# Kernel optimization log

Hardware: AMD Instinct MI355X
Metric: run time of the kernel (lower is better)

Reference implementation:

```python
import jax, jax.numpy as jnp
import numpy as np
import math

B, S, D, H = 4, 512, 128, 4
HD = D // H
NEG = float(-2**32 + 1)

def _ln(x, g, b, eps=1e-8):
    m = jnp.mean(x, axis=-1, keepdims=True)
    v = jnp.var(x, axis=-1, keepdims=True)
    return (x - m) * jax.lax.rsqrt(v + eps) * g + b

def setup_inputs() -> dict:
    key = jax.random.key(0)
    ks = jax.random.split(key, 16)
    s = 0.02
    inp = {
        'embed': jax.random.normal(ks[0], (B, S, D), jnp.float32),
        'time_matrix_K': jax.random.normal(ks[1], (B, S, S, D), jnp.float32),
        'time_matrix_V': jax.random.normal(ks[2], (B, S, S, D), jnp.float32),
        # causal additive mask: large negative above diagonal (1--mask semantics)
        'attn_mask': jnp.where(jnp.triu(jnp.ones((S, S), bool), k=1), jnp.float32(-1e9), jnp.float32(0.0)),
        'padding_mask': jnp.zeros((B, S), bool),
        'wq': jax.random.normal(ks[3], (D, D), jnp.float32) * s,
        'bq': jnp.zeros((D,), jnp.float32),
        'wk': jax.random.normal(ks[4], (D, D), jnp.float32) * s,
        'bk': jnp.zeros((D,), jnp.float32),
        'wv': jax.random.normal(ks[5], (D, D), jnp.float32) * s,
        'bv': jnp.zeros((D,), jnp.float32),
        'wo': jax.random.normal(ks[6], (D, D), jnp.float32) * s,
        'bo': jnp.zeros((D,), jnp.float32),
        'ln1_g': jnp.ones((D,), jnp.float32),
        'ln1_b': jnp.zeros((D,), jnp.float32),
        'ln2_g': jnp.ones((D,), jnp.float32),
        'ln2_b': jnp.zeros((D,), jnp.float32),
        'w1': jax.random.normal(ks[7], (D, D), jnp.float32) * s,  # d_ff defaults to d_model
        'b1': jnp.zeros((D,), jnp.float32),
        'w2': jax.random.normal(ks[8], (D, D), jnp.float32) * s,
        'b2': jnp.zeros((D,), jnp.float32),
    }
    return inp

def reference(embed, time_matrix_K, time_matrix_V, attn_mask, padding_mask,
              wq, bq, wk, bk, wv, bv, wo, bo,
              ln1_g, ln1_b, ln2_g, ln2_b, w1, b1, w2, b2):
    # Pre-LN on Q only (K, V take raw embed), per original block
    Qn = _ln(embed, ln1_g, ln1_b)
    q = (Qn @ wq + bq).reshape(B, S, H, HD).transpose(0, 2, 1, 3)      # bhqd
    k = (embed @ wk + bk).reshape(B, S, H, HD).transpose(0, 2, 1, 3)   # bhkd
    v = (embed @ wv + bv).reshape(B, S, H, HD).transpose(0, 2, 1, 3)   # bhkd
    tmK = time_matrix_K.reshape(B, S, S, H, HD).transpose(0, 3, 1, 2, 4)  # bhqkd
    tmV = time_matrix_V.reshape(B, S, S, H, HD).transpose(0, 3, 1, 2, 4)  # bhqkd
    scale = math.sqrt(HD)
    energy = jnp.einsum('bhqd,bhkd->bhqk', q, k)
    energy = energy + jnp.einsum('bhqkd,bhqd->bhqk', tmK, q)
    energy = energy / scale
    energy = energy + attn_mask[None, None]
    energy = jnp.where(padding_mask[:, None, None, :], jnp.float32(NEG), energy)
    attn = jax.nn.softmax(energy, axis=-1)  # dropout is identity in eval
    O = jnp.einsum('bhqk,bhkd->bhqd', attn, v)
    O = O + jnp.einsum('bhqk,bhqkd->bhqd', attn, tmV)
    O = O.transpose(0, 2, 1, 3).reshape(B, S, D)
    O = O @ wo + bo
    x = Qn + O                      # residual adds LN'd Q, per original code
    x = _ln(x, ln2_g, ln2_b)
    ff = jax.nn.gelu(x @ w1 + b1, approximate=False) @ w2 + b2
    return ff + x
```

## Files before the change

### kernel.cpp

```cpp
#include <hip/hip_runtime.h>
#include <math.h>

#define Bsz 4
#define Ssz 512
#define Dsz 128
#define Hsz 4
#define HDsz 32
#define KT 64
#define NT 8

typedef float floatx4 __attribute__((ext_vector_type(4)));

static __device__ __forceinline__ float4 ldnt4(const float* p) {
    floatx4 v = __builtin_nontemporal_load(reinterpret_cast<const floatx4*>(p));
    float4 r; r.x = v.x; r.y = v.y; r.z = v.z; r.w = v.w;
    return r;
}

__global__ __launch_bounds__(128) void k_pre(
    const float* __restrict__ embed,
    const float* __restrict__ wq, const float* __restrict__ bq,
    const float* __restrict__ wk, const float* __restrict__ bk,
    const float* __restrict__ wv, const float* __restrict__ bv,
    const float* __restrict__ g1, const float* __restrict__ b1,
    float* __restrict__ Qn, float* __restrict__ Qs,
    float* __restrict__ Kp, float* __restrict__ Vp)
{
    __shared__ float xs[4][128];
    __shared__ float qs[4][128];
    const int t = threadIdx.x;
    const int row0 = blockIdx.x * 4;
    const int r = t >> 5;
    const int c = t & 31;
    const int d4 = c << 2;

    const float4* e4 = (const float4*)(embed + (size_t)row0 * Dsz);
    float4 x4 = e4[r * 32 + c];

    float s = x4.x + x4.y + x4.z + x4.w;
    #pragma unroll
    for (int o = 1; o < 32; o <<= 1) s += __shfl_xor(s, o);
    const float m = s * (1.0f / 128.0f);

    const float dx0 = x4.x - m, dx1 = x4.y - m, dx2 = x4.z - m, dx3 = x4.w - m;
    float vs = dx0*dx0 + dx1*dx1 + dx2*dx2 + dx3*dx3;
    #pragma unroll
    for (int o = 1; o < 32; o <<= 1) vs += __shfl_xor(vs, o);
    const float rstd = rsqrtf(vs * (1.0f / 128.0f) + 1e-8f);

    const float4 g4 = *(const float4*)(g1 + d4);
    const float4 bb4 = *(const float4*)(b1 + d4);
    float4 qn4;
    qn4.x = dx0 * rstd * g4.x + bb4.x;
    qn4.y = dx1 * rstd * g4.y + bb4.y;
    qn4.z = dx2 * rstd * g4.z + bb4.z;
    qn4.w = dx3 * rstd * g4.w + bb4.w;

    xs[r][d4+0] = x4.x; xs[r][d4+1] = x4.y; xs[r][d4+2] = x4.z; xs[r][d4+3] = x4.w;
    qs[r][d4+0] = qn4.x; qs[r][d4+1] = qn4.y; qs[r][d4+2] = qn4.z; qs[r][d4+3] = qn4.w;
    *(float4*)(Qn + (size_t)(row0 + r) * Dsz + d4) = qn4;
    __syncthreads();

    float aq[4] = {0,0,0,0}, ak[4] = {0,0,0,0}, av[4] = {0,0,0,0};
    for (int d = 0; d < 128; ++d) {
        const float wqv = wq[d*128 + t];
        const float wkv = wk[d*128 + t];
        const float wvv = wv[d*128 + t];
        #pragma unroll
        for (int rr = 0; rr < 4; ++rr) {
            aq[rr] += qs[rr][d] * wqv;
            ak[rr] += xs[rr][d] * wkv;
            av[rr] += xs[rr][d] * wvv;
        }
    }
    const float inv_scale = 0.17677669529663687f;
    const float bqv = bq[t], bkv = bk[t], bvv = bv[t];
    #pragma unroll
    for (int rr = 0; rr < 4; ++rr) {
        const size_t o = (size_t)(row0 + rr) * Dsz + t;
        Qs[o] = (aq[rr] + bqv) * inv_scale;
        Kp[o] = ak[rr] + bkv;
        Vp[o] = av[rr] + bvv;
    }
}

__global__ __launch_bounds__(256) void k_attn_tile(
    const float* __restrict__ tmK, const float* __restrict__ tmV,
    const float* __restrict__ Qs, const float* __restrict__ Kp,
    const float* __restrict__ Vp,
    float* __restrict__ Opart,
    float* __restrict__ ml)
{
    const int id = blockIdx.x;
    const int b = id & 3;
    const int q = (id >> 2) & (Ssz - 1);
    const int tile = id >> 11;
    const int k0 = tile * KT;
    if (k0 > q) return;

    const int t = threadIdx.x;
    const int w = t >> 6;
    const int lane = t & 63;
    const int rg = lane >> 3;
    const int fs = lane & 7;
    const int d4 = w * HDsz + fs * 4;

    const int nr_full = q - k0 + 1;
    const int nr = nr_full > KT ? KT : nr_full;
    const size_t rowq = (size_t)(b * Ssz + q);

    const float4 q4 = *(const float4*)(Qs + rowq * Dsz + d4);
    const float* tmKb = tmK + (rowq * (size_t)Ssz + k0) * Dsz;
    const float* Kb   = Kp + ((size_t)b * Ssz + k0) * Dsz;

    float p[8];
    #pragma unroll
    for (int i0 = 0; i0 < 8; i0 += 4) {
        float4 a[4], kv[4];
        #pragma unroll
        for (int u = 0; u < 4; ++u) {
            const int r = (i0 + u) * 8 + rg;
            if (r < nr) {
                a[u]  = ldnt4(tmKb + (size_t)r * Dsz + d4);
                kv[u] = *(const float4*)(Kb + (size_t)r * Dsz + d4);
            } else {
                a[u] = make_float4(0,0,0,0); kv[u] = make_float4(0,0,0,0);
            }
        }
        #pragma unroll
        for (int u = 0; u < 4; ++u) {
            const int r = (i0 + u) * 8 + rg;
            float val = q4.x*(a[u].x+kv[u].x) + q4.y*(a[u].y+kv[u].y)
                      + q4.z*(a[u].z+kv[u].z) + q4.w*(a[u].w+kv[u].w);
            val += __shfl_xor(val, 1);
            val += __shfl_xor(val, 2);
            val += __shfl_xor(val, 4);
            p[i0 + u] = (r < nr) ? val : -INFINITY;
        }
    }

    float mx = p[0];
    #pragma unroll
    for (int i = 1; i < 8; ++i) mx = fmaxf(mx, p[i]);
    mx = fmaxf(mx, __shfl_xor(mx, 8));
    mx = fmaxf(mx, __shfl_xor(mx, 16));
    mx = fmaxf(mx, __shfl_xor(mx, 32));

    float lsum = 0.0f;
    #pragma unroll
    for (int i = 0; i < 8; ++i) {
        p[i] = __expf(p[i] - mx);
        lsum += p[i];
    }
    lsum += __shfl_xor(lsum, 8);
    lsum += __shfl_xor(lsum, 16);
    lsum += __shfl_xor(lsum, 32);

    if (lane == 0) {
        float* mlp = ml + ((rowq * NT + tile) * Hsz + w) * 2;
        mlp[0] = mx;
        mlp[1] = lsum;
    }

    const float* tmVb = tmV + (rowq * (size_t)Ssz + k0) * Dsz;
    const float* Vb   = Vp + ((size_t)b * Ssz + k0) * Dsz;
    float4 acc = {0.0f, 0.0f, 0.0f, 0.0f};
    #pragma unroll
    for (int i0 = 0; i0 < 8; i0 += 4) {
        float4 a[4], vv[4];
        #pragma unroll
        for (int u = 0; u < 4; ++u) {
            const int r = (i0 + u) * 8 + rg;
            if (r < nr) {
                a[u]  = ldnt4(tmVb + (size_t)r * Dsz + d4);
                vv[u] = *(const float4*)(Vb + (size_t)r * Dsz + d4);
            } else {
                a[u] = make_float4(0,0,0,0); vv[u] = make_float4(0,0,0,0);
            }
        }
        #pragma unroll
        for (int u = 0; u < 4; ++u) {
            const float pw = p[i0 + u];
            acc.x += pw * (a[u].x + vv[u].x);
            acc.y += pw * (a[u].y + vv[u].y);
            acc.z += pw * (a[u].z + vv[u].z);
            acc.w += pw * (a[u].w + vv[u].w);
        }
    }
    #pragma unroll
    for (int o = 8; o < 64; o <<= 1) {
        acc.x += __shfl_xor(acc.x, o);
        acc.y += __shfl_xor(acc.y, o);
        acc.z += __shfl_xor(acc.z, o);
        acc.w += __shfl_xor(acc.w, o);
    }
    if (lane < 8) {
        float4* op = (float4*)(Opart + (rowq * NT + tile) * Dsz + d4);
        *op = acc;
    }
}

__global__ __launch_bounds__(128) void k_combine(
    const float* __restrict__ Opart, const float* __restrict__ ml,
    float* __restrict__ Oa)
{
    const size_t rowq = blockIdx.x;
    const int q = (int)(rowq & (Ssz - 1));
    const int nt = (q >> 6) + 1;
    const int d = threadIdx.x;
    const int h = d >> 5;

    float M = -INFINITY;
    #pragma unroll 8
    for (int i = 0; i < nt; ++i)
        M = fmaxf(M, ml[((rowq * NT + i) * Hsz + h) * 2 + 0]);

    float den = 0.0f, o = 0.0f;
    #pragma unroll 8
    for (int i = 0; i < nt; ++i) {
        const float* mlp = ml + ((rowq * NT + i) * Hsz + h) * 2;
        const float w = __expf(mlp[0] - M);
        den += w * mlp[1];
        o   += w * Opart[(rowq * NT + i) * Dsz + d];
    }
    Oa[rowq * Dsz + d] = o / den;
}

__global__ __launch_bounds__(128) void k_post(
    const float* __restrict__ Oa, const float* __restrict__ Qn,
    const float* __restrict__ wo, const float* __restrict__ bo,
    const float* __restrict__ g2, const float* __restrict__ b2ln,
    const float* __restrict__ w1, const float* __restrict__ b1,
    const float* __restrict__ w2, const float* __restrict__ b2,
    float* __restrict__ out)
{
    __shared__ float os[4][128];
    __shared__ float xn[4][128];
    __shared__ float hbuf[4][128];
    const int t = threadIdx.x;
    const int row0 = blockIdx.x * 4;
    const int r = t >> 5;
    const int c = t & 31;
    const int d4 = c << 2;

    {
        const float4* o4 = (const float4*)(Oa + (size_t)row0 * Dsz);
        const float4 v = o4[r * 32 + c];
        os[r][d4+0] = v.x; os[r][d4+1] = v.y; os[r][d4+2] = v.z; os[r][d4+3] = v.w;
    }
    __syncthreads();

    float ao[4] = {0,0,0,0};
    for (int d = 0; d < 128; ++d) {
        const float wv = wo[d*128 + t];
        #pragma unroll
        for (int rr = 0; rr < 4; ++rr) ao[rr] += os[rr][d] * wv;
    }
    const float bov = bo[t];
    float xrow[4];
    #pragma unroll
    for (int rr = 0; rr < 4; ++rr)
        xrow[rr] = Qn[(size_t)(row0 + rr) * Dsz + t] + ao[rr] + bov;
    __syncthreads();
    #pragma unroll
    for (int rr = 0; rr < 4; ++rr) os[rr][t] = xrow[rr];
    __syncthreads();

    {
        const float4 x4 = *(const float4*)(&os[r][d4]);
        float s = x4.x + x4.y + x4.z + x4.w;
        #pragma unroll
        for (int o = 1; o < 32; o <<= 1) s += __shfl_xor(s, o);
        const float m = s * (1.0f / 128.0f);
        const float dx0 = x4.x - m, dx1 = x4.y - m, dx2 = x4.z - m, dx3 = x4.w - m;
        float vs = dx0*dx0 + dx1*dx1 + dx2*dx2 + dx3*dx3;
        #pragma unroll
        for (int o = 1; o < 32; o <<= 1) vs += __shfl_xor(vs, o);
        const float rstd = rsqrtf(vs * (1.0f / 128.0f) + 1e-8f);
        const float4 g4 = *(const float4*)(g2 + d4);
        const float4 bb4 = *(const float4*)(b2ln + d4);
        xn[r][d4+0] = dx0 * rstd * g4.x + bb4.x;
        xn[r][d4+1] = dx1 * rstd * g4.y + bb4.y;
        xn[r][d4+2] = dx2 * rstd * g4.z + bb4.z;
        xn[r][d4+3] = dx3 * rstd * g4.w + bb4.w;
    }
    __syncthreads();

    float a1[4] = {0,0,0,0};
    for (int d = 0; d < 128; ++d) {
        const float wv = w1[d*128 + t];
        #pragma unroll
        for (int rr = 0; rr < 4; ++rr) a1[rr] += xn[rr][d] * wv;
    }
    const float b1v = b1[t];
    #pragma unroll
    for (int rr = 0; rr < 4; ++rr) {
        const float hv = a1[rr] + b1v;
        hbuf[rr][t] = 0.5f * hv * (1.0f + erff(hv * 0.70710678118654752f));
    }
    __syncthreads();

    float a2[4] = {0,0,0,0};
    for (int d = 0; d < 128; ++d) {
        const float wv = w2[d*128 + t];
        #pragma unroll
        for (int rr = 0; rr < 4; ++rr) a2[rr] += hbuf[rr][d] * wv;
    }
    const float b2v = b2[t];
    #pragma unroll
    for (int rr = 0; rr < 4; ++rr)
        out[(size_t)(row0 + rr) * Dsz + t] = a2[rr] + b2v + xn[rr][t];
}

extern "C" void kernel_launch(void* const* d_in, const int* in_sizes, int n_in,
                              void* d_out, int out_size, void* d_ws, size_t ws_size,
                              hipStream_t stream) {
    const float* embed = (const float*)d_in[0];
    const float* tmK   = (const float*)d_in[1];
    const float* tmV   = (const float*)d_in[2];
    const float* wq = (const float*)d_in[5];
    const float* bq = (const float*)d_in[6];
    const float* wk = (const float*)d_in[7];
    const float* bk = (const float*)d_in[8];
    const float* wv = (const float*)d_in[9];
    const float* bv = (const float*)d_in[10];
    const float* wo = (const float*)d_in[11];
    const float* bo = (const float*)d_in[12];
    const float* g1 = (const float*)d_in[13];
    const float* b1l = (const float*)d_in[14];
    const float* g2 = (const float*)d_in[15];
    const float* b2l = (const float*)d_in[16];
    const float* w1 = (const float*)d_in[17];
    const float* b1 = (const float*)d_in[18];
    const float* w2 = (const float*)d_in[19];
    const float* b2 = (const float*)d_in[20];

    const size_t NE = (size_t)Bsz * Ssz * Dsz;
    float* ws = (float*)d_ws;
    float* Qn = ws;
    float* Qs = ws + NE;
    float* Kp = ws + 2 * NE;
    float* Vp = ws + 3 * NE;
    float* Oa = ws + 4 * NE;
    float* Opart = ws + 5 * NE;
    float* mlbuf = ws + 5 * NE + (size_t)Bsz * Ssz * NT * Dsz;

    k_pre<<<(Bsz * Ssz) / 4, 128, 0, stream>>>(embed, wq, bq, wk, bk, wv, bv,
                                               g1, b1l, Qn, Qs, Kp, Vp);
    k_attn_tile<<<Bsz * Ssz * NT, 256, 0, stream>>>(tmK, tmV, Qs, Kp, Vp,
                                                    Opart, mlbuf);
    k_combine<<<Bsz * Ssz, 128, 0, stream>>>(Opart, mlbuf, Oa);
    k_post<<<(Bsz * Ssz) / 4, 128, 0, stream>>>(Oa, Qn, wo, bo, g2, b2l,
                                                w1, b1, w2, b2, (float*)d_out);
}
```

Measured before the change: 141.6 us.

## Remap attention tiles to one wave each and fuse split-K combine into post kernel

Each wave now handles a whole (query, key-tile) pair covering all four heads, with lanes spanning the 128-wide feature row and two rows in flight. This lengthens per-lane row loops, adds a fast path with no bounds checks for full tiles, and cuts cross-lane reductions. The separate combine kernel is removed and its log-sum-exp merge moves into k_post, which saves one launch and the Oa round trip. The trade-off is higher register pressure from p[32] and 8-deep load batches, and an early return per wave inside a block could leave idle waves.

```diff
diff --git a/kernel.cpp b/kernel.cpp
--- a/kernel.cpp
+++ b/kernel.cpp
@@ -84,26 +84,24 @@
     }
 }
 
-__global__ __launch_bounds__(256) void k_attn_tile(
+__global__ __launch_bounds__(256, 4) void k_attn_tile(
     const float* __restrict__ tmK, const float* __restrict__ tmV,
     const float* __restrict__ Qs, const float* __restrict__ Kp,
     const float* __restrict__ Vp,
     float* __restrict__ Opart,
     float* __restrict__ ml)
 {
-    const int id = blockIdx.x;
-    const int b = id & 3;
-    const int q = (id >> 2) & (Ssz - 1);
-    const int tile = id >> 11;
+    const int tau = blockIdx.x * 4 + (threadIdx.x >> 6);
+    const int b = tau & 3;
+    const int q = (tau >> 2) & (Ssz - 1);
+    const int tile = tau >> 11;
     const int k0 = tile * KT;
     if (k0 > q) return;
 
-    const int t = threadIdx.x;
-    const int w = t >> 6;
-    const int lane = t & 63;
-    const int rg = lane >> 3;
-    const int fs = lane & 7;
-    const int d4 = w * HDsz + fs * 4;
+    const int lane = threadIdx.x & 63;
+    const int r5 = lane >> 5;
+    const int fs = lane & 31;
+    const int d4 = fs << 2;
 
     const int nr_full = q - k0 + 1;
     const int nr = nr_full > KT ? KT : nr_full;
@@ -113,51 +111,70 @@
     const float* tmKb = tmK + (rowq * (size_t)Ssz + k0) * Dsz;
     const float* Kb   = Kp + ((size_t)b * Ssz + k0) * Dsz;
 
-    float p[8];
-    #pragma unroll
-    for (int i0 = 0; i0 < 8; i0 += 4) {
-        float4 a[4], kv[4];
-        #pragma unroll
-        for (int u = 0; u < 4; ++u) {
-            const int r = (i0 + u) * 8 + rg;
-            if (r < nr) {
-                a[u]  = ldnt4(tmKb + (size_t)r * Dsz + d4);
-                kv[u] = *(const float4*)(Kb + (size_t)r * Dsz + d4);
-            } else {
-                a[u] = make_float4(0,0,0,0); kv[u] = make_float4(0,0,0,0);
-            }
-        }
-        #pragma unroll
-        for (int u = 0; u < 4; ++u) {
-            const int r = (i0 + u) * 8 + rg;
-            float val = q4.x*(a[u].x+kv[u].x) + q4.y*(a[u].y+kv[u].y)
-                      + q4.z*(a[u].z+kv[u].z) + q4.w*(a[u].w+kv[u].w);
-            val += __shfl_xor(val, 1);
-            val += __shfl_xor(val, 2);
-            val += __shfl_xor(val, 4);
-            p[i0 + u] = (r < nr) ? val : -INFINITY;
+    float p[32];
+
+    if (nr == KT) {
+        #pragma unroll
+        for (int c2 = 0; c2 < 4; ++c2) {
+            float4 a[8], kv[8];
+            #pragma unroll
+            for (int jj = 0; jj < 8; ++jj) {
+                const int r = 2*(c2*8 + jj) + r5;
+                a[jj]  = ldnt4(tmKb + (size_t)r * Dsz + d4);
+                kv[jj] = *(const float4*)(Kb + (size_t)r * Dsz + d4);
+            }
+            #pragma unroll
+            for (int jj = 0; jj < 8; ++jj) {
+                float val = q4.x*(a[jj].x+kv[jj].x) + q4.y*(a[jj].y+kv[jj].y)
+                          + q4.z*(a[jj].z+kv[jj].z) + q4.w*(a[jj].w+kv[jj].w);
+                val += __shfl_xor(val, 1);
+                val += __shfl_xor(val, 2);
+                val += __shfl_xor(val, 4);
+                p[c2*8 + jj] = val;
+            }
+        }
+    } else {
+        #pragma unroll
+        for (int c2 = 0; c2 < 4; ++c2) {
+            float4 a[8], kv[8];
+            #pragma unroll
+            for (int jj = 0; jj < 8; ++jj) {
+                const int r = 2*(c2*8 + jj) + r5;
+                if (r < nr) {
+                    a[jj]  = ldnt4(tmKb + (size_t)r * Dsz + d4);
+                    kv[jj] = *(const float4*)(Kb + (size_t)r * Dsz + d4);
+                } else {
+                    a[jj] = make_float4(0,0,0,0); kv[jj] = make_float4(0,0,0,0);
+                }
+            }
+            #pragma unroll
+            for (int jj = 0; jj < 8; ++jj) {
+                const int r = 2*(c2*8 + jj) + r5;
+                float val = q4.x*(a[jj].x+kv[jj].x) + q4.y*(a[jj].y+kv[jj].y)
+                          + q4.z*(a[jj].z+kv[jj].z) + q4.w*(a[jj].w+kv[jj].w);
+                val += __shfl_xor(val, 1);
+                val += __shfl_xor(val, 2);
+                val += __shfl_xor(val, 4);
+                p[c2*8 + jj] = (r < nr) ? val : -INFINITY;
+            }
         }
     }
 
     float mx = p[0];
     #pragma unroll
-    for (int i = 1; i < 8; ++i) mx = fmaxf(mx, p[i]);
-    mx = fmaxf(mx, __shfl_xor(mx, 8));
-    mx = fmaxf(mx, __shfl_xor(mx, 16));
+    for (int i = 1; i < 32; ++i) mx = fmaxf(mx, p[i]);
     mx = fmaxf(mx, __shfl_xor(mx, 32));
 
     float lsum = 0.0f;
     #pragma unroll
-    for (int i = 0; i < 8; ++i) {
+    for (int i = 0; i < 32; ++i) {
         p[i] = __expf(p[i] - mx);
         lsum += p[i];
     }
-    lsum += __shfl_xor(lsum, 8);
-    lsum += __shfl_xor(lsum, 16);
     lsum += __shfl_xor(lsum, 32);
 
-    if (lane == 0) {
-        float* mlp = ml + ((rowq * NT + tile) * Hsz + w) * 2;
+    if (r5 == 0 && (fs & 7) == 0) {
+        float* mlp = ml + ((rowq * NT + tile) * Hsz + (fs >> 3)) * 2;
         mlp[0] = mx;
         mlp[1] = lsum;
     }
@@ -165,69 +182,62 @@
     const float* tmVb = tmV + (rowq * (size_t)Ssz + k0) * Dsz;
     const float* Vb   = Vp + ((size_t)b * Ssz + k0) * Dsz;
     float4 acc = {0.0f, 0.0f, 0.0f, 0.0f};
-    #pragma unroll
-    for (int i0 = 0; i0 < 8; i0 += 4) {
-        float4 a[4], vv[4];
-        #pragma unroll
-        for (int u = 0; u < 4; ++u) {
-            const int r = (i0 + u) * 8 + rg;
-            if (r < nr) {
-                a[u]  = ldnt4(tmVb + (size_t)r * Dsz + d4);
-                vv[u] = *(const float4*)(Vb + (size_t)r * Dsz + d4);
-            } else {
-                a[u] = make_float4(0,0,0,0); vv[u] = make_float4(0,0,0,0);
-            }
-        }
-        #pragma unroll
-        for (int u = 0; u < 4; ++u) {
-            const float pw = p[i0 + u];
-            acc.x += pw * (a[u].x + vv[u].x);
-            acc.y += pw * (a[u].y + vv[u].y);
-            acc.z += pw * (a[u].z + vv[u].z);
-            acc.w += pw * (a[u].w + vv[u].w);
-        }
-    }
-    #pragma unroll
-    for (int o = 8; o < 64; o <<= 1) {
-        acc.x += __shfl_xor(acc.x, o);
-        acc.y += __shfl_xor(acc.y, o);
-        acc.z += __shfl_xor(acc.z, o);
-        acc.w += __shfl_xor(acc.w, o);
-    }
-    if (lane < 8) {
+    if (nr == KT) {
+        #pragma unroll
+        for (int c2 = 0; c2 < 4; ++c2) {
+            float4 a[8], vv[8];
+            #pragma unroll
+            for (int jj = 0; jj < 8; ++jj) {
+                const int r = 2*(c2*8 + jj) + r5;
+                a[jj]  = ldnt4(tmVb + (size_t)r * Dsz + d4);
+                vv[jj] = *(const float4*)(Vb + (size_t)r * Dsz + d4);
+            }
+            #pragma unroll
+            for (int jj = 0; jj < 8; ++jj) {
+                const float pw = p[c2*8 + jj];
+                acc.x += pw * (a[jj].x + vv[jj].x);
+                acc.y += pw * (a[jj].y + vv[jj].y);
+                acc.z += pw * (a[jj].z + vv[jj].z);
+                acc.w += pw * (a[jj].w + vv[jj].w);
+            }
+        }
+    } else {
+        #pragma unroll
+        for (int c2 = 0; c2 < 4; ++c2) {
+            float4 a[8], vv[8];
+            #pragma unroll
+            for (int jj = 0; jj < 8; ++jj) {
+                const int r = 2*(c2*8 + jj) + r5;
+                if (r < nr) {
+                    a[jj]  = ldnt4(tmVb + (size_t)r * Dsz + d4);
+                    vv[jj] = *(const float4*)(Vb + (size_t)r * Dsz + d4);
+                } else {
+                    a[jj] = make_float4(0,0,0,0); vv[jj] = make_float4(0,0,0,0);
+                }
+            }
+            #pragma unroll
+            for (int jj = 0; jj < 8; ++jj) {
+                const float pw = p[c2*8 + jj];
+                acc.x += pw * (a[jj].x + vv[jj].x);
+                acc.y += pw * (a[jj].y + vv[jj].y);
+                acc.z += pw * (a[jj].z + vv[jj].z);
+                acc.w += pw * (a[jj].w + vv[jj].w);
+            }
+        }
+    }
+    acc.x += __shfl_xor(acc.x, 32);
+    acc.y += __shfl_xor(acc.y, 32);
+    acc.z += __shfl_xor(acc.z, 32);
+    acc.w += __shfl_xor(acc.w, 32);
+    if (lane < 32) {
         float4* op = (float4*)(Opart + (rowq * NT + tile) * Dsz + d4);
         *op = acc;
     }
 }
 
-__global__ __launch_bounds__(128) void k_combine(
+__global__ __launch_bounds__(128) void k_post(
     const float* __restrict__ Opart, const float* __restrict__ ml,
-    float* __restrict__ Oa)
-{
-    const size_t rowq = blockIdx.x;
-    const int q = (int)(rowq & (Ssz - 1));
-    const int nt = (q >> 6) + 1;
-    const int d = threadIdx.x;
-    const int h = d >> 5;
-
-    float M = -INFINITY;
-    #pragma unroll 8
-    for (int i = 0; i < nt; ++i)
-        M = fmaxf(M, ml[((rowq * NT + i) * Hsz + h) * 2 + 0]);
-
-    float den = 0.0f, o = 0.0f;
-    #pragma unroll 8
-    for (int i = 0; i < nt; ++i) {
-        const float* mlp = ml + ((rowq * NT + i) * Hsz + h) * 2;
-        const float w = __expf(mlp[0] - M);
-        den += w * mlp[1];
-        o   += w * Opart[(rowq * NT + i) * Dsz + d];
-    }
-    Oa[rowq * Dsz + d] = o / den;
-}
-
-__global__ __launch_bounds__(128) void k_post(
-    const float* __restrict__ Oa, const float* __restrict__ Qn,
+    const float* __restrict__ Qn,
     const float* __restrict__ wo, const float* __restrict__ bo,
     const float* __restrict__ g2, const float* __restrict__ b2ln,
     const float* __restrict__ w1, const float* __restrict__ b1,
@@ -242,11 +252,24 @@
     const int r = t >> 5;
     const int c = t & 31;
     const int d4 = c << 2;
-
-    {
-        const float4* o4 = (const float4*)(Oa + (size_t)row0 * Dsz);
-        const float4 v = o4[r * 32 + c];
-        os[r][d4+0] = v.x; os[r][d4+1] = v.y; os[r][d4+2] = v.z; os[r][d4+3] = v.w;
+    const int h = t >> 5;
+
+    #pragma unroll
+    for (int rr = 0; rr < 4; ++rr) {
+        const size_t rowq = (size_t)(row0 + rr);
+        const int q = (int)(rowq & (Ssz - 1));
+        const int nt = (q >> 6) + 1;
+        float M = -INFINITY;
+        for (int i = 0; i < nt; ++i)
+            M = fmaxf(M, ml[((rowq * NT + i) * Hsz + h) * 2 + 0]);
+        float den = 0.0f, o = 0.0f;
+        for (int i = 0; i < nt; ++i) {
+            const float* mlp = ml + ((rowq * NT + i) * Hsz + h) * 2;
+            const float w = __expf(mlp[0] - M);
+            den += w * mlp[1];
+            o   += w * Opart[(rowq * NT + i) * Dsz + t];
+        }
+        os[rr][t] = o / den;
     }
     __syncthreads();
 
@@ -341,15 +364,14 @@
     float* Qs = ws + NE;
     float* Kp = ws + 2 * NE;
     float* Vp = ws + 3 * NE;
-    float* Oa = ws + 4 * NE;
-    float* Opart = ws + 5 * NE;
-    float* mlbuf = ws + 5 * NE + (size_t)Bsz * Ssz * NT * Dsz;
+    float* Opart = ws + 4 * NE;
+    float* mlbuf = ws + 4 * NE + (size_t)Bsz * Ssz * NT * Dsz;
 
     k_pre<<<(Bsz * Ssz) / 4, 128, 0, stream>>>(embed, wq, bq, wk, bk, wv, bv,
                                                g1, b1l, Qn, Qs, Kp, Vp);
-    k_attn_tile<<<Bsz * Ssz * NT, 256, 0, stream>>>(tmK, tmV, Qs, Kp, Vp,
-                                                    Opart, mlbuf);
-    k_combine<<<Bsz * Ssz, 128, 0, stream>>>(Opart, mlbuf, Oa);
-    k_post<<<(Bsz * Ssz) / 4, 128, 0, stream>>>(Oa, Qn, wo, bo, g2, b2l,
-                                                w1, b1, w2, b2, (float*)d_out);
-}
+    k_attn_tile<<<(Bsz * Ssz * NT) / 4, 256, 0, stream>>>(tmK, tmV, Qs, Kp, Vp,
+                                                          Opart, mlbuf);
+    k_post<<<(Bsz * Ssz) / 4, 128, 0, stream>>>(Opart, mlbuf, Qn, wo, bo,
+                                                g2, b2l, w1, b1, w2, b2,
+                                                (float*)d_out);
+}
```

Result: slower. 309.0 us (+118.2%).
